# Kernel tuning notes

Measured on AMD Instinct MI355X. Metric: run time of the kernel, lower is better.

## Reference

```python
import jax, jax.numpy as jnp
import numpy as np

B, L, D, H = 4, 1024, 768, 12
HD = D // H
MAXREL = 2  # hardcoded self.max_relative_position = 2 in the module


def rel_index(l):
    # index matrix into the (2*MAXREL+1, HD) relative embedding table
    r = jnp.arange(l)
    dist = r[None, :] - r[:, None]          # [l, l] = k - q
    return jnp.clip(dist, -MAXREL, MAXREL) + MAXREL


def setup_inputs() -> dict:
    key = jax.random.key(0)
    ks = jax.random.split(key, 8)

    def xavier(k, shape):
        fan_out, fan_in = shape[0], shape[1]
        lim = (6.0 / (fan_in + fan_out)) ** 0.5
        return jax.random.uniform(k, shape, jnp.float32, -lim, lim)

    return {
        "x": jax.random.normal(ks[0], (B, L, D), jnp.float32),
        "Wq": xavier(ks[1], (D, D)), "bq": jnp.zeros((D,), jnp.float32),
        "Wk": xavier(ks[2], (D, D)), "bk": jnp.zeros((D,), jnp.float32),
        "Wv": xavier(ks[3], (D, D)), "bv": jnp.zeros((D,), jnp.float32),
        "Wo": xavier(ks[4], (D, D)), "bo": jnp.zeros((D,), jnp.float32),
        "rel_k": xavier(ks[5], (2 * MAXREL + 1, HD)),
        "rel_v": xavier(ks[6], (2 * MAXREL + 1, HD)),
    }


def reference(x, Wq, bq, Wk, bk, Wv, bv, Wo, bo, rel_k, rel_v):
    b, l, d = x.shape
    h, hd = H, HD
    scale = d ** (-0.5)  # NOTE: module DIVIDES by dim**-0.5, i.e. multiplies by sqrt(dim). Faithful.

    q_ = x @ Wq.T + bq
    k_ = x @ Wk.T + bk
    v_ = x @ Wv.T + bv

    # torch's permute/view head split is equivalent to the standard (h outer) split
    q = q_.reshape(b, l, h, hd).transpose(0, 2, 1, 3)  # [b,h,l,hd]
    k = k_.reshape(b, l, h, hd).transpose(0, 2, 1, 3)
    v = v_.reshape(b, l, h, hd).transpose(0, 2, 1, 3)

    attn1 = jnp.einsum("bhqd,bhkd->bhqk", q, k)

    idx = rel_index(l)        # [l,l] int
    rk = rel_k[idx]           # [l,l,hd]
    attn2 = jnp.einsum("bhqd,qkd->bhqk", q, rk)

    attn = jax.nn.softmax((attn1 + attn2) / scale, axis=-1)  # dropout = identity (eval)

    w1 = jnp.einsum("bhqk,bhkd->bhqd", attn, v)
    rv = rel_v[idx]           # [l,l,hd]
    w2 = jnp.einsum("bhqk,qkd->bhqd", attn, rv)

    out = (w1 + w2).transpose(0, 2, 1, 3).reshape(b, l, d)
    out = out @ Wo.T + bo     # multi_head_dropout = identity (eval)
    return out, attn
```

## Files before the change

### kernel.cpp

```cpp
#include <hip/hip_runtime.h>
#include <hip/hip_bf16.h>

#define DD    768
#define NH    12
#define HDIM  64
#define LSEQ  1024
#define NB    4
#define SCALE 27.712812921102035f

typedef __attribute__((ext_vector_type(8))) short bf16x8;
typedef __attribute__((ext_vector_type(4))) float f32x4;

__device__ __forceinline__ ushort bf16_rne(float f) {
    uint u = __float_as_uint(f);
    return (ushort)((u + 0x7FFFu + ((u >> 16) & 1u)) >> 16);
}
__device__ __forceinline__ float bf16_tof(ushort h) {
    return __uint_as_float(((uint)h) << 16);
}
__device__ __forceinline__ void split4(const float4 v, ushort4& h, ushort4& l) {
#pragma unroll
    for (int c = 0; c < 4; c++) {
        const float f  = (&v.x)[c];
        const ushort hb = bf16_rne(f);
        (&h.x)[c] = hb;
        (&l.x)[c] = bf16_rne(f - bf16_tof(hb));
    }
}

__device__ __forceinline__ void swz3(int& bx, int& by, int& bz) {
    const int gx = gridDim.x, gy = gridDim.y;
    const int nwg = gx * gy * gridDim.z;
    int flat = blockIdx.x + gx * (blockIdx.y + gy * blockIdx.z);
    flat = (flat & 7) * (nwg >> 3) + (flat >> 3);
    bx = flat % gx; const int t = flat / gx; by = t % gy; bz = t / gy;
}

template<bool HAS_BIAS>
__device__ __forceinline__ void mfma_core(
        const float* __restrict__ A, int lda, int m0,
        const float* __restrict__ B, int ldb, int n0,
        float* __restrict__ C, int ldc,
        const float* __restrict__ bias, int K)
{
    __shared__ __align__(16) ushort Ah[128][40];
    __shared__ __align__(16) ushort Al[128][40];
    __shared__ __align__(16) ushort Bh[128][40];
    __shared__ __align__(16) ushort Bl[128][40];

    const int tid  = threadIdx.x;
    const int lane = tid & 63;
    const int wid  = tid >> 6;
    const int wr   = wid >> 1;
    const int wc   = wid & 1;
    const int lrow = lane & 15;
    const int lkg  = lane >> 4;

    const int sr = tid >> 3;
    const int sc = (tid & 7) * 4;

    f32x4 acc[4][4];
#pragma unroll
    for (int i = 0; i < 4; i++)
#pragma unroll
        for (int j = 0; j < 4; j++)
#pragma unroll
            for (int e = 0; e < 4; e++) acc[i][j][e] = 0.f;

    for (int k0 = 0; k0 < K; k0 += 32) {
        float4 av[4], bv[4];
#pragma unroll
        for (int p = 0; p < 4; p++) {
            const int row = p * 32 + sr;
            av[p] = *(const float4*)&A[(size_t)(m0 + row) * lda + k0 + sc];
            bv[p] = *(const float4*)&B[(size_t)(n0 + row) * ldb + k0 + sc];
        }
        __syncthreads();
#pragma unroll
        for (int p = 0; p < 4; p++) {
            const int row = p * 32 + sr;
            ushort4 h4, l4;
            split4(av[p], h4, l4);
            *(ushort4*)&Ah[row][sc] = h4;
            *(ushort4*)&Al[row][sc] = l4;
            split4(bv[p], h4, l4);
            *(ushort4*)&Bh[row][sc] = h4;
            *(ushort4*)&Bl[row][sc] = l4;
        }
        __syncthreads();

        bf16x8 fah[4], fal[4], fbh[4], fbl[4];
#pragma unroll
        for (int t = 0; t < 4; t++) {
            fah[t] = *(const bf16x8*)&Ah[wr * 64 + t * 16 + lrow][lkg * 8];
            fal[t] = *(const bf16x8*)&Al[wr * 64 + t * 16 + lrow][lkg * 8];
            fbh[t] = *(const bf16x8*)&Bh[wc * 64 + t * 16 + lrow][lkg * 8];
            fbl[t] = *(const bf16x8*)&Bl[wc * 64 + t * 16 + lrow][lkg * 8];
        }
#pragma unroll
        for (int i = 0; i < 4; i++)
#pragma unroll
            for (int j = 0; j < 4; j++) {
                acc[i][j] = __builtin_amdgcn_mfma_f32_16x16x32_bf16(fah[i], fbh[j], acc[i][j], 0, 0, 0);
                acc[i][j] = __builtin_amdgcn_mfma_f32_16x16x32_bf16(fah[i], fbl[j], acc[i][j], 0, 0, 0);
                acc[i][j] = __builtin_amdgcn_mfma_f32_16x16x32_bf16(fal[i], fbh[j], acc[i][j], 0, 0, 0);
            }
    }

#pragma unroll
    for (int j = 0; j < 4; j++) {
        const int col = n0 + wc * 64 + j * 16 + lrow;
        const float badd = HAS_BIAS ? bias[col] : 0.f;
#pragma unroll
        for (int i = 0; i < 4; i++) {
            const int rbase = m0 + wr * 64 + i * 16 + lkg * 4;
#pragma unroll
            for (int e = 0; e < 4; e++)
                C[(size_t)(rbase + e) * ldc + col] = acc[i][j][e] + badd;
        }
    }
}

__global__ __launch_bounds__(256) void mfma_qkv(
        const float* __restrict__ x,
        const float* __restrict__ W0, const float* __restrict__ c0, float* __restrict__ O0,
        const float* __restrict__ W1, const float* __restrict__ c1, float* __restrict__ O1,
        const float* __restrict__ W2, const float* __restrict__ c2, float* __restrict__ O2) {
    int bx, by, bz; swz3(bx, by, bz);
    const float* W; const float* bias; float* C;
    if      (bz == 0) { W = W0; bias = c0; C = O0; }
    else if (bz == 1) { W = W1; bias = c1; C = O1; }
    else              { W = W2; bias = c2; C = O2; }
    mfma_core<true>(x, DD, by * 128, W, DD, bx * 128, C, DD, bias, DD);
}

__global__ __launch_bounds__(256) void mfma_proj(
        const float* __restrict__ A, const float* __restrict__ W,
        const float* __restrict__ bias, float* __restrict__ C) {
    int bx, by, bz; swz3(bx, by, bz);
    mfma_core<true>(A, DD, by * 128, W, DD, bx * 128, C, DD, bias, DD);
}

__global__ __launch_bounds__(256) void mfma_logits(
        const float* __restrict__ Q, const float* __restrict__ Kp,
        float* __restrict__ Sout) {
    int bx, by, bz; swz3(bx, by, bz);
    const int b = bz / NH, h = bz % NH;
    const float* Ab = Q  + (size_t)b * LSEQ * DD + h * HDIM;
    const float* Bb = Kp + (size_t)b * LSEQ * DD + h * HDIM;
    float* Cb = Sout + ((size_t)bz << 20);
    mfma_core<false>(Ab, DD, by * 128, Bb, DD, bx * 128, Cb, LSEQ, nullptr, HDIM);
}

__global__ __launch_bounds__(256) void softmax_kernel(
        const float* __restrict__ Q, const float* __restrict__ rel_k,
        float* __restrict__ attn, float* __restrict__ coef) {
    __shared__ float relk[5][64];
    __shared__ float cstash[4][8];

    const int tid  = threadIdx.x;
    const int wave = tid >> 6;
    const int lane = tid & 63;
    const int row_global = blockIdx.x * 4 + wave;
    const int bh = row_global >> 10;
    const int q  = row_global & (LSEQ - 1);
    const int b  = bh / NH;
    const int h  = bh % NH;

    for (int i = tid; i < 5 * HDIM; i += 256)
        relk[i >> 6][i & 63] = rel_k[i];
    if (lane < 8) cstash[wave][lane] = 0.f;
    __syncthreads();

    const float qv = Q[((size_t)b * LSEQ + q) * DD + h * HDIM + lane];
    float qr[5];
#pragma unroll
    for (int j = 0; j < 5; j++) {
        float t = qv * relk[j][lane];
#pragma unroll
        for (int off = 32; off; off >>= 1) t += __shfl_xor(t, off);
        qr[j] = t;
    }

    float* rowp = attn + ((size_t)row_global << 10);

    float lg[16];
    float m = -1e30f;
#pragma unroll
    for (int i = 0; i < 4; i++) {
        float4 x = *(const float4*)&rowp[i*256 + lane*4];
#pragma unroll
        for (int c = 0; c < 4; c++) {
            const int k  = i*256 + lane*4 + c;
            const int dk = k - q;
            const int bkt = (dk < -2 ? -2 : (dk > 2 ? 2 : dk)) + 2;
            const float val = ((&x.x)[c] + qr[bkt]) * SCALE;
            lg[i*4 + c] = val;
            m = fmaxf(m, val);
        }
    }
#pragma unroll
    for (int off = 32; off; off >>= 1) m = fmaxf(m, __shfl_xor(m, off));

    float tot = 0.f, lft = 0.f, rgt = 0.f;
#pragma unroll
    for (int e = 0; e < 16; e++) {
        const int k = (e >> 2) * 256 + lane*4 + (e & 3);
        const float p = __expf(lg[e] - m);
        lg[e] = p;
        tot += p;
        if (k <= q - 2) lft += p;
        if (k >= q + 2) rgt += p;
    }
#pragma unroll
    for (int off = 32; off; off >>= 1) {
        tot += __shfl_xor(tot, off);
        lft += __shfl_xor(lft, off);
        rgt += __shfl_xor(rgt, off);
    }
    const float inv = 1.0f / tot;

#pragma unroll
    for (int i = 0; i < 4; i++) {
        float4 o;
#pragma unroll
        for (int c = 0; c < 4; c++) {
            const int k = i*256 + lane*4 + c;
            const float p = lg[i*4 + c] * inv;
            (&o.x)[c] = p;
            if (k == q - 1) cstash[wave][1] = p;
            if (k == q    ) cstash[wave][2] = p;
            if (k == q + 1) cstash[wave][3] = p;
        }
        *(float4*)&rowp[i*256 + lane*4] = o;
    }
    __syncthreads();

    if (lane == 0) {
        float* cp = coef + (size_t)row_global * 8;
        cp[0] = lft * inv;
        cp[1] = cstash[wave][1];
        cp[2] = cstash[wave][2];
        cp[3] = cstash[wave][3];
        cp[4] = rgt * inv;
    }
}

__global__ __launch_bounds__(256) void pv_kernel(
        const float* __restrict__ attn, const float* __restrict__ V,
        const float* __restrict__ coef, const float* __restrict__ rel_v,
        float* __restrict__ ctx) {
    __shared__ __align__(16) float Ps_t[64][68];
    __shared__ __align__(16) float Vs[64][68];
    __shared__ float relv[5][64];
    __shared__ float cf[64][5];

    int bx, by, bz; swz3(bx, by, bz);
    const int tid = threadIdx.x;
    const int tx  = tid & 15;
    const int ty  = tid >> 4;
    const int bh  = by;
    const int m0  = bx * 64;
    const int b   = bh / NH;
    const int h   = bh % NH;

    const float* P  = attn + ((size_t)bh << 20) + (size_t)m0 * LSEQ;
    const float* Vb = V + (size_t)b * LSEQ * DD + (size_t)h * HDIM;

    for (int i = tid; i < 5 * HDIM; i += 256)
        relv[i >> 6][i & 63] = rel_v[i];
    for (int i = tid; i < 64 * 5; i += 256) {
        const int r = i / 5, j = i % 5;
        cf[r][j] = coef[((size_t)bh * LSEQ + m0 + r) * 8 + j];
    }

    float acc[4][4];
#pragma unroll
    for (int i = 0; i < 4; i++)
#pragma unroll
        for (int j = 0; j < 4; j++) acc[i][j] = 0.f;

    for (int k0 = 0; k0 < LSEQ; k0 += 64) {
        float4 pv[4], vv[4];
#pragma unroll
        for (int t = 0; t < 4; t++) {
            const int linear = t*256 + tid;
            const int row  = linear >> 4;
            const int col4 = (linear & 15) * 4;
            pv[t] = *(const float4*)&P[(size_t)row * LSEQ + k0 + col4];
            vv[t] = *(const float4*)&Vb[(size_t)(k0 + row) * DD + col4];
        }
        __syncthreads();
#pragma unroll
        for (int t = 0; t < 4; t++) {
            const int linear = t*256 + tid;
            const int row  = linear >> 4;
            const int col4 = (linear & 15) * 4;
#pragma unroll
            for (int c = 0; c < 4; c++)
                Ps_t[col4 + c][row] = (&pv[t].x)[c];
            *(float4*)&Vs[row][col4] = vv[t];
        }
        __syncthreads();
#pragma unroll
        for (int kk = 0; kk < 64; kk++) {
            float4 pa = *(const float4*)&Ps_t[kk][ty * 4];
            float4 vw = *(const float4*)&Vs[kk][tx * 4];
#pragma unroll
            for (int i = 0; i < 4; i++)
#pragma unroll
                for (int j = 0; j < 4; j++)
                    acc[i][j] = fmaf((&pa.x)[i], (&vw.x)[j], acc[i][j]);
        }
    }

#pragma unroll
    for (int i = 0; i < 4; i++) {
        const int r = ty * 4 + i;
        float4 o;
#pragma unroll
        for (int j = 0; j < 4; j++) {
            float v = acc[i][j];
#pragma unroll
            for (int jb = 0; jb < 5; jb++)
                v = fmaf(cf[r][jb], relv[jb][tx * 4 + j], v);
            (&o.x)[j] = v;
        }
        *(float4*)&ctx[((size_t)b * LSEQ + m0 + r) * DD + h * HDIM + tx * 4] = o;
    }
}

extern "C" void kernel_launch(void* const* d_in, const int* in_sizes, int n_in,
                              void* d_out, int out_size, void* d_ws, size_t ws_size,
                              hipStream_t stream) {
    const float* x     = (const float*)d_in[0];
    const float* Wq    = (const float*)d_in[1];
    const float* bq    = (const float*)d_in[2];
    const float* Wk    = (const float*)d_in[3];
    const float* bk    = (const float*)d_in[4];
    const float* Wv    = (const float*)d_in[5];
    const float* bv    = (const float*)d_in[6];
    const float* Wo    = (const float*)d_in[7];
    const float* bo    = (const float*)d_in[8];
    const float* rel_k = (const float*)d_in[9];
    const float* rel_v = (const float*)d_in[10];

    float* out  = (float*)d_out;
    float* attn = out + (size_t)NB * LSEQ * DD;

    const size_t n_tok = (size_t)NB * LSEQ * DD;
    float* Q    = (float*)d_ws;
    float* Kp   = Q   + n_tok;
    float* Vp   = Kp  + n_tok;
    float* coef = Vp  + n_tok;
    float* ctx  = Q;

    dim3 g1(DD / 128, (NB * LSEQ) / 128, 3);
    mfma_qkv<<<g1, 256, 0, stream>>>(x, Wq, bq, Q, Wk, bk, Kp, Wv, bv, Vp);

    dim3 g2(LSEQ / 128, LSEQ / 128, NB * NH);
    mfma_logits<<<g2, 256, 0, stream>>>(Q, Kp, attn);

    dim3 g3(NB * NH * LSEQ / 4);
    softmax_kernel<<<g3, 256, 0, stream>>>(Q, rel_k, attn, coef);

    dim3 g4(LSEQ / 64, NB * NH);
    pv_kernel<<<g4, 256, 0, stream>>>(attn, Vp, coef, rel_v, ctx);

    dim3 g5(DD / 128, (NB * LSEQ) / 128, 1);
    mfma_proj<<<g5, 256, 0, stream>>>(ctx, Wo, bo, out);
}
```

Baseline: 554.0 us.

## Rewrite attention-times-V kernel with split-bf16 MFMA and 128-row tiles

Replaces the scalar FP32 FMA P·V kernel with one that splits P and V into high and low bf16 parts and runs three bf16 MFMA products per tile, keeping close to FP32 accuracy. The query tile grows from 64 to 128 rows and the K step shrinks to 32, with V transposed into shared memory. The aim is to take the P·V matmul off the vector ALUs and onto the matrix units. The cost is extra conversion and shared-memory work, a grid half the size (384 blocks), and scalar rather than vectorized ctx stores.

```diff
diff --git a/kernel.cpp b/kernel.cpp
--- a/kernel.cpp
+++ b/kernel.cpp
@@ -246,87 +246,120 @@
     }
 }
 
-__global__ __launch_bounds__(256) void pv_kernel(
+__global__ __launch_bounds__(256) void pv_mfma(
         const float* __restrict__ attn, const float* __restrict__ V,
         const float* __restrict__ coef, const float* __restrict__ rel_v,
         float* __restrict__ ctx) {
-    __shared__ __align__(16) float Ps_t[64][68];
-    __shared__ __align__(16) float Vs[64][68];
+    __shared__ __align__(16) ushort Ph[128][40];
+    __shared__ __align__(16) ushort Pl[128][40];
+    __shared__ __align__(16) ushort Vth[64][40];
+    __shared__ __align__(16) ushort Vtl[64][40];
     __shared__ float relv[5][64];
-    __shared__ float cf[64][5];
+    __shared__ float cf[128][5];
 
     int bx, by, bz; swz3(bx, by, bz);
-    const int tid = threadIdx.x;
-    const int tx  = tid & 15;
-    const int ty  = tid >> 4;
-    const int bh  = by;
-    const int m0  = bx * 64;
-    const int b   = bh / NH;
-    const int h   = bh % NH;
+    const int tid  = threadIdx.x;
+    const int lane = tid & 63;
+    const int wid  = tid >> 6;
+    const int wr   = wid >> 1;
+    const int wc   = wid & 1;
+    const int lrow = lane & 15;
+    const int lkg  = lane >> 4;
+
+    const int bh = by;
+    const int m0 = bx * 128;
+    const int b  = bh / NH;
+    const int h  = bh % NH;
 
     const float* P  = attn + ((size_t)bh << 20) + (size_t)m0 * LSEQ;
     const float* Vb = V + (size_t)b * LSEQ * DD + (size_t)h * HDIM;
 
     for (int i = tid; i < 5 * HDIM; i += 256)
         relv[i >> 6][i & 63] = rel_v[i];
-    for (int i = tid; i < 64 * 5; i += 256) {
+    for (int i = tid; i < 128 * 5; i += 256) {
         const int r = i / 5, j = i % 5;
         cf[r][j] = coef[((size_t)bh * LSEQ + m0 + r) * 8 + j];
     }
 
-    float acc[4][4];
+    const int sr = tid >> 3;
+    const int sc = (tid & 7) * 4;
+    const int vr = tid >> 4;
+    const int vc = (tid & 15) * 4;
+
+    f32x4 acc[4][2];
 #pragma unroll
     for (int i = 0; i < 4; i++)
 #pragma unroll
-        for (int j = 0; j < 4; j++) acc[i][j] = 0.f;
-
-    for (int k0 = 0; k0 < LSEQ; k0 += 64) {
-        float4 pv[4], vv[4];
+        for (int j = 0; j < 2; j++)
+#pragma unroll
+            for (int e = 0; e < 4; e++) acc[i][j][e] = 0.f;
+
+    for (int k0 = 0; k0 < LSEQ; k0 += 32) {
+        float4 pv4[4], vv[2];
+#pragma unroll
+        for (int p = 0; p < 4; p++)
+            pv4[p] = *(const float4*)&P[(size_t)(p * 32 + sr) * LSEQ + k0 + sc];
+#pragma unroll
+        for (int p = 0; p < 2; p++)
+            vv[p] = *(const float4*)&Vb[(size_t)(k0 + p * 16 + vr) * DD + vc];
+        __syncthreads();
+#pragma unroll
+        for (int p = 0; p < 4; p++) {
+            ushort4 h4, l4;
+            split4(pv4[p], h4, l4);
+            *(ushort4*)&Ph[p * 32 + sr][sc] = h4;
+            *(ushort4*)&Pl[p * 32 + sr][sc] = l4;
+        }
+#pragma unroll
+        for (int p = 0; p < 2; p++) {
+            ushort4 h4, l4;
+            split4(vv[p], h4, l4);
+            const int krow = p * 16 + vr;
+#pragma unroll
+            for (int c = 0; c < 4; c++) {
+                Vth[vc + c][krow] = (&h4.x)[c];
+                Vtl[vc + c][krow] = (&l4.x)[c];
+            }
+        }
+        __syncthreads();
+
+        bf16x8 pah[4], pal[4], vbh[2], vbl[2];
 #pragma unroll
         for (int t = 0; t < 4; t++) {
-            const int linear = t*256 + tid;
-            const int row  = linear >> 4;
-            const int col4 = (linear & 15) * 4;
-            pv[t] = *(const float4*)&P[(size_t)row * LSEQ + k0 + col4];
-            vv[t] = *(const float4*)&Vb[(size_t)(k0 + row) * DD + col4];
-        }
-        __syncthreads();
-#pragma unroll
-        for (int t = 0; t < 4; t++) {
-            const int linear = t*256 + tid;
-            const int row  = linear >> 4;
-            const int col4 = (linear & 15) * 4;
-#pragma unroll
-            for (int c = 0; c < 4; c++)
-                Ps_t[col4 + c][row] = (&pv[t].x)[c];
-            *(float4*)&Vs[row][col4] = vv[t];
-        }
-        __syncthreads();
-#pragma unroll
-        for (int kk = 0; kk < 64; kk++) {
-            float4 pa = *(const float4*)&Ps_t[kk][ty * 4];
-            float4 vw = *(const float4*)&Vs[kk][tx * 4];
-#pragma unroll
-            for (int i = 0; i < 4; i++)
-#pragma unroll
-                for (int j = 0; j < 4; j++)
-                    acc[i][j] = fmaf((&pa.x)[i], (&vw.x)[j], acc[i][j]);
-        }
-    }
-
-#pragma unroll
-    for (int i = 0; i < 4; i++) {
-        const int r = ty * 4 + i;
-        float4 o;
-#pragma unroll
-        for (int j = 0; j < 4; j++) {
-            float v = acc[i][j];
-#pragma unroll
-            for (int jb = 0; jb < 5; jb++)
-                v = fmaf(cf[r][jb], relv[jb][tx * 4 + j], v);
-            (&o.x)[j] = v;
-        }
-        *(float4*)&ctx[((size_t)b * LSEQ + m0 + r) * DD + h * HDIM + tx * 4] = o;
+            pah[t] = *(const bf16x8*)&Ph[wr * 64 + t * 16 + lrow][lkg * 8];
+            pal[t] = *(const bf16x8*)&Pl[wr * 64 + t * 16 + lrow][lkg * 8];
+        }
+#pragma unroll
+        for (int t = 0; t < 2; t++) {
+            vbh[t] = *(const bf16x8*)&Vth[wc * 32 + t * 16 + lrow][lkg * 8];
+            vbl[t] = *(const bf16x8*)&Vtl[wc * 32 + t * 16 + lrow][lkg * 8];
+        }
+#pragma unroll
+        for (int i = 0; i < 4; i++)
+#pragma unroll
+            for (int j = 0; j < 2; j++) {
+                acc[i][j] = __builtin_amdgcn_mfma_f32_16x16x32_bf16(pah[i], vbh[j], acc[i][j], 0, 0, 0);
+                acc[i][j] = __builtin_amdgcn_mfma_f32_16x16x32_bf16(pah[i], vbl[j], acc[i][j], 0, 0, 0);
+                acc[i][j] = __builtin_amdgcn_mfma_f32_16x16x32_bf16(pal[i], vbh[j], acc[i][j], 0, 0, 0);
+            }
+    }
+
+#pragma unroll
+    for (int j = 0; j < 2; j++) {
+        const int dcol = wc * 32 + j * 16 + lrow;
+#pragma unroll
+        for (int i = 0; i < 4; i++) {
+            const int qb = wr * 64 + i * 16 + lkg * 4;
+#pragma unroll
+            for (int e = 0; e < 4; e++) {
+                const int qloc = qb + e;
+                float v = acc[i][j][e];
+#pragma unroll
+                for (int jb = 0; jb < 5; jb++)
+                    v = fmaf(cf[qloc][jb], relv[jb][dcol], v);
+                ctx[((size_t)(b * LSEQ + m0 + qloc)) * DD + h * HDIM + dcol] = v;
+            }
+        }
     }
 }
 
@@ -364,8 +397,8 @@
     dim3 g3(NB * NH * LSEQ / 4);
     softmax_kernel<<<g3, 256, 0, stream>>>(Q, rel_k, attn, coef);
 
-    dim3 g4(LSEQ / 64, NB * NH);
-    pv_kernel<<<g4, 256, 0, stream>>>(attn, Vp, coef, rel_v, ctx);
+    dim3 g4(LSEQ / 128, NB * NH);
+    pv_mfma<<<g4, 256, 0, stream>>>(attn, Vp, coef, rel_v, ctx);
 
     dim3 g5(DD / 128, (NB * LSEQ) / 128, 1);
     mfma_proj<<<g5, 256, 0, stream>>>(ctx, Wo, bo, out);
```

Result: faster. 514.5 us (-7.1%).
